# Kernel tuning notes

Measured on AMD Instinct MI355X. Metric: run time of the kernel, lower is better.

## Reference

```python
import jax, jax.numpy as jnp
import numpy as np

N = 50000      # nodes
E = 800000     # edges
F_IN = 128     # num_features
H = 64         # hidden_dim
G = 64         # graphs in batch
EPS = 1e-5


def setup_inputs() -> dict:
    ks = jax.random.split(jax.random.key(0), 16)
    x = jax.random.normal(ks[0], (N, F_IN), dtype=jnp.float32)
    edge_index = jax.random.randint(ks[1], (2, E), 0, N, dtype=jnp.int64)
    batch = jnp.sort(jax.random.randint(ks[2], (N,), 0, G, dtype=jnp.int64))
    s = 0.05
    inp = {"x": x, "edge_index": edge_index, "batch": batch}
    # GCNConv layers: W [out,in], bias [out]; BatchNorm gamma/beta [H]
    dims = [(H, F_IN), (H, H), (H, H)]
    for i, (o, ci) in enumerate(dims):
        inp[f"W{i}"] = jax.random.normal(ks[3 + i], (o, ci), dtype=jnp.float32) * s
        inp[f"b{i}"] = jnp.zeros((o,), dtype=jnp.float32)
        inp[f"g{i}"] = jnp.ones((o,), dtype=jnp.float32)
        inp[f"be{i}"] = jnp.zeros((o,), dtype=jnp.float32)
    inp["lin1_w"] = jax.random.normal(ks[10], (H // 2, H), dtype=jnp.float32) * s
    inp["lin1_b"] = jnp.zeros((H // 2,), dtype=jnp.float32)
    inp["lin2_w"] = jax.random.normal(ks[11], (1, H // 2), dtype=jnp.float32) * s
    inp["lin2_b"] = jnp.zeros((1,), dtype=jnp.float32)
    return inp


def _gcn_conv(x, src, dst, W, b):
    # PyG GCNConv: h = x W^T; add self-loops; symmetric deg^{-1/2} norm; scatter-add; + bias
    h = x @ W.T                                   # [N, out]
    n = x.shape[0]
    deg = jax.ops.segment_sum(jnp.ones(src.shape[0], h.dtype), dst, num_segments=n) + 1.0
    dinv = jax.lax.rsqrt(deg)                     # [N]
    msg = h[src] * (dinv[src] * dinv[dst])[:, None]   # per-edge messages
    agg = jax.ops.segment_sum(msg, dst, num_segments=n)
    agg = agg + h * (dinv * dinv)[:, None]        # self-loop contribution
    return agg + b


def _bn_relu(x, g, be):
    # BatchNorm1d (training-mode batch stats, biased var) + ReLU; dropout = identity (eval)
    m = x.mean(axis=0)
    v = jnp.var(x, axis=0)
    return jax.nn.relu((x - m) * jax.lax.rsqrt(v + EPS) * g + be)


def reference(x, edge_index, batch,
              W0, b0, g0, be0, W1, b1, g1, be1, W2, b2, g2, be2,
              lin1_w, lin1_b, lin2_w, lin2_b):
    src, dst = edge_index[0], edge_index[1]
    Ws = [(W0, b0, g0, be0), (W1, b1, g1, be1), (W2, b2, g2, be2)]
    h = x
    for (W, b, g, be) in Ws:
        h = _bn_relu(_gcn_conv(h, src, dst, W, b), g, be)
    # global mean pool over graphs
    sums = jax.ops.segment_sum(h, batch, num_segments=G)          # [G, H]
    cnt = jax.ops.segment_sum(jnp.ones((h.shape[0],), h.dtype), batch, num_segments=G)
    pooled = sums / jnp.maximum(cnt, 1.0)[:, None]
    h = jax.nn.relu(pooled @ lin1_w.T + lin1_b)
    return h @ lin2_w.T + lin2_b                                   # [G, 1]
```

## Files before the change

### kernel.cpp

```cpp
#include <hip/hip_runtime.h>

#define NN 50000
#define NE 800000
#define FIN 128
#define H 64
#define NG 64
#define BN_EPS 1e-5f
#define INV_N (1.0f / 50000.0f)
#define NBKT 196

__global__ void setup_misc(const float* __restrict__ W0, const float* __restrict__ W1,
                           const float* __restrict__ W2, float* __restrict__ Wt0,
                           float* __restrict__ Wt1, float* __restrict__ Wt2,
                           float* __restrict__ sl0, float* __restrict__ sl1,
                           float* __restrict__ sl2, float* __restrict__ poolcnt,
                           int* __restrict__ bktcnt) {
    int i = blockIdx.x * 256 + threadIdx.x;
    if (i < 64 * 128) { sl0[i] = 0.f; sl1[i] = 0.f; sl2[i] = 0.f; }
    if (i < NG * H + NG) poolcnt[i] = 0.f;
    if (i < NBKT) bktcnt[i] = 0;
    if (i < FIN * 64) {
        int k = i >> 6, o = i & 63;
        Wt0[i] = W0[o * FIN + k];
    }
    if (i < H * 64) {
        int k = i >> 6, o = i & 63;
        Wt1[i] = W1[o * H + k];
        Wt2[i] = W2[o * H + k];
    }
}

__global__ void bucket_hist(const int* __restrict__ dst, int* __restrict__ bktcnt, int E) {
    __shared__ int cnt[NBKT];
    const int chunk = (E + gridDim.x - 1) / gridDim.x;
    const int e0 = blockIdx.x * chunk;
    const int e1 = min(e0 + chunk, E);
    for (int i = threadIdx.x; i < NBKT; i += 256) cnt[i] = 0;
    __syncthreads();
    for (int e = e0 + threadIdx.x; e < e1; e += 256) atomicAdd(&cnt[dst[e] >> 8], 1);
    __syncthreads();
    for (int i = threadIdx.x; i < NBKT; i += 256)
        if (cnt[i]) atomicAdd(&bktcnt[i], cnt[i]);
}

__global__ void bucket_scan(const int* __restrict__ bktcnt, int* __restrict__ bb,
                            int* __restrict__ bcur, int E) {
    __shared__ int s[256];
    int v = (threadIdx.x < NBKT) ? bktcnt[threadIdx.x] : 0;
    s[threadIdx.x] = v;
    __syncthreads();
    for (int off = 1; off < 256; off <<= 1) {
        int t = (threadIdx.x >= off) ? s[threadIdx.x - off] : 0;
        __syncthreads();
        s[threadIdx.x] += t;
        __syncthreads();
    }
    if (threadIdx.x < NBKT) {
        int base = s[threadIdx.x] - v;
        bb[threadIdx.x] = base;
        bcur[threadIdx.x] = base;
    }
    if (threadIdx.x == 0) bb[NBKT] = E;
}

__global__ void bin_edges(const int* __restrict__ src, const int* __restrict__ dst,
                          int* __restrict__ bcur, unsigned int* __restrict__ staged, int E) {
    __shared__ int cnt[NBKT];
    __shared__ int offs[NBKT];
    const int chunk = (E + gridDim.x - 1) / gridDim.x;
    const int e0 = blockIdx.x * chunk;
    const int e1 = min(e0 + chunk, E);
    for (int i = threadIdx.x; i < NBKT; i += 256) cnt[i] = 0;
    __syncthreads();
    for (int e = e0 + threadIdx.x; e < e1; e += 256) atomicAdd(&cnt[dst[e] >> 8], 1);
    __syncthreads();
    for (int i = threadIdx.x; i < NBKT; i += 256) {
        int c = cnt[i];
        offs[i] = c ? atomicAdd(&bcur[i], c) : 0;
        cnt[i] = 0;
    }
    __syncthreads();
    for (int e = e0 + threadIdx.x; e < e1; e += 256) {
        int d = dst[e];
        int bkt = d >> 8;
        int idx = atomicAdd(&cnt[bkt], 1);
        staged[offs[bkt] + idx] = (unsigned int)src[e] | ((unsigned int)(d & 255) << 16);
    }
}

__global__ void csr_build(const unsigned int* __restrict__ staged, const int* __restrict__ bb,
                          int* __restrict__ row_start, float* __restrict__ dinv,
                          int* __restrict__ csr_src, int n, int E) {
    __shared__ int cnt[256];
    __shared__ int loc[256];
    __shared__ int cur[256];
    const int b = blockIdx.x;
    cnt[threadIdx.x] = 0;
    __syncthreads();
    const int e0 = bb[b], e1 = bb[b + 1];
    for (int e = e0 + threadIdx.x; e < e1; e += 256)
        atomicAdd(&cnt[(staged[e] >> 16) & 255], 1);
    __syncthreads();
    int v = cnt[threadIdx.x];
    loc[threadIdx.x] = v;
    __syncthreads();
    for (int off = 1; off < 256; off <<= 1) {
        int t = (threadIdx.x >= off) ? loc[threadIdx.x - off] : 0;
        __syncthreads();
        loc[threadIdx.x] += t;
        __syncthreads();
    }
    const int start = e0 + loc[threadIdx.x] - v;
    const int node = b * 256 + threadIdx.x;
    if (node < n) {
        row_start[node] = start;
        dinv[node] = rsqrtf((float)v + 1.0f);
    }
    if (node == n) row_start[n] = E;
    cur[threadIdx.x] = start;
    __syncthreads();
    for (int e = e0 + threadIdx.x; e < e1; e += 256) {
        unsigned int u = staged[e];
        int j = atomicAdd(&cur[(u >> 16) & 255], 1);
        csr_src[j] = (int)(u & 0xFFFFu);
    }
}

template <int K>
__global__ __launch_bounds__(256, 4) void matmul_tile(const float* __restrict__ x,
                                                      const float* __restrict__ Wtg,
                                                      const float* __restrict__ st,
                                                      const float* __restrict__ gamma,
                                                      const float* __restrict__ beta,
                                                      float* __restrict__ out, int n) {
    __shared__ float Xs[64 * 68];
    __shared__ float Ws[64 * 64];
    const int base = blockIdx.x * 64;
    const int q = threadIdx.x >> 4;
    const int co = (threadIdx.x & 15) * 4;

    float4 a0 = make_float4(0.f, 0.f, 0.f, 0.f);
    float4 a1 = a0, a2 = a0, a3 = a0;

    for (int kc = 0; kc < K; kc += 64) {
        if (kc) __syncthreads();
        for (int i = threadIdx.x; i < 64 * 64; i += 256) Ws[i] = Wtg[kc * 64 + i];
        {
            const int kq = (threadIdx.x & 15) * 4;
            float4 sc = make_float4(1.f, 1.f, 1.f, 1.f);
            float4 sh = make_float4(0.f, 0.f, 0.f, 0.f);
            if (st) {
                int kk = kc + kq;
                float4 s = *(const float4*)&st[kk];
                float4 ss = *(const float4*)&st[64 + kk];
                float4 gm = *(const float4*)&gamma[kk];
                float4 bt = *(const float4*)&beta[kk];
                float mx = s.x * INV_N, my = s.y * INV_N, mz = s.z * INV_N, mw = s.w * INV_N;
                sc.x = gm.x * rsqrtf(ss.x * INV_N - mx * mx + BN_EPS);
                sc.y = gm.y * rsqrtf(ss.y * INV_N - my * my + BN_EPS);
                sc.z = gm.z * rsqrtf(ss.z * INV_N - mz * mz + BN_EPS);
                sc.w = gm.w * rsqrtf(ss.w * INV_N - mw * mw + BN_EPS);
                sh.x = bt.x - mx * sc.x;
                sh.y = bt.y - my * sc.y;
                sh.z = bt.z - mz * sc.z;
                sh.w = bt.w - mw * sc.w;
            }
            for (int j = 0; j < 4; ++j) {
                int r = (threadIdx.x >> 4) + j * 16;
                int row = base + r;
                float4 v = make_float4(0.f, 0.f, 0.f, 0.f);
                if (row < n) v = *(const float4*)&x[(size_t)row * K + kc + kq];
                if (st) {
                    v.x = fmaxf(v.x * sc.x + sh.x, 0.f);
                    v.y = fmaxf(v.y * sc.y + sh.y, 0.f);
                    v.z = fmaxf(v.z * sc.z + sh.z, 0.f);
                    v.w = fmaxf(v.w * sc.w + sh.w, 0.f);
                }
                *(float4*)&Xs[r * 68 + kq] = v;
            }
        }
        __syncthreads();

#pragma unroll 2
        for (int k = 0; k < 64; k += 4) {
            float4 x0 = *(const float4*)&Xs[(q + 0) * 68 + k];
            float4 x1 = *(const float4*)&Xs[(q + 16) * 68 + k];
            float4 x2 = *(const float4*)&Xs[(q + 32) * 68 + k];
            float4 x3 = *(const float4*)&Xs[(q + 48) * 68 + k];
            float4 w0 = *(const float4*)&Ws[(k + 0) * 64 + co];
            float4 w1 = *(const float4*)&Ws[(k + 1) * 64 + co];
            float4 w2 = *(const float4*)&Ws[(k + 2) * 64 + co];
            float4 w3 = *(const float4*)&Ws[(k + 3) * 64 + co];

            a0.x += x0.x * w0.x + x0.y * w1.x + x0.z * w2.x + x0.w * w3.x;
            a0.y += x0.x * w0.y + x0.y * w1.y + x0.z * w2.y + x0.w * w3.y;
            a0.z += x0.x * w0.z + x0.y * w1.z + x0.z * w2.z + x0.w * w3.z;
            a0.w += x0.x * w0.w + x0.y * w1.w + x0.z * w2.w + x0.w * w3.w;

            a1.x += x1.x * w0.x + x1.y * w1.x + x1.z * w2.x + x1.w * w3.x;
            a1.y += x1.x * w0.y + x1.y * w1.y + x1.z * w2.y + x1.w * w3.y;
            a1.z += x1.x * w0.z + x1.y * w1.z + x1.z * w2.z + x1.w * w3.z;
            a1.w += x1.x * w0.w + x1.y * w1.w + x1.z * w2.w + x1.w * w3.w;

            a2.x += x2.x * w0.x + x2.y * w1.x + x2.z * w2.x + x2.w * w3.x;
            a2.y += x2.x * w0.y + x2.y * w1.y + x2.z * w2.y + x2.w * w3.y;
            a2.z += x2.x * w0.z + x2.y * w1.z + x2.z * w2.z + x2.w * w3.z;
            a2.w += x2.x * w0.w + x2.y * w1.w + x2.z * w2.w + x2.w * w3.w;

            a3.x += x3.x * w0.x + x3.y * w1.x + x3.z * w2.x + x3.w * w3.x;
            a3.y += x3.x * w0.y + x3.y * w1.y + x3.z * w2.y + x3.w * w3.y;
            a3.z += x3.x * w0.z + x3.y * w1.z + x3.z * w2.z + x3.w * w3.z;
            a3.w += x3.x * w0.w + x3.y * w1.w + x3.z * w2.w + x3.w * w3.w;
        }
    }

    int r0 = base + q;
    if (r0 < n) *(float4*)&out[(size_t)r0 * H + co] = a0;
    if (r0 + 16 < n) *(float4*)&out[(size_t)(r0 + 16) * H + co] = a1;
    if (r0 + 32 < n) *(float4*)&out[(size_t)(r0 + 32) * H + co] = a2;
    if (r0 + 48 < n) *(float4*)&out[(size_t)(r0 + 48) * H + co] = a3;
}

__global__ void gcn_gather(const float* __restrict__ h, const int* __restrict__ row_start,
                           const int* __restrict__ csr_src, const float* __restrict__ dinv,
                           const float* __restrict__ bias, float* __restrict__ out,
                           float* __restrict__ slots, int n) {
    const int wv = threadIdx.x >> 6;
    const int c = threadIdx.x & 63;
    const int d0 = blockIdx.x * 8 + wv * 2;
    float vA = 0.f, vB = 0.f;
    if (d0 < n) {
        const int d1 = d0 + 1;
        int jA = row_start[d0];
        const int jm = row_start[d1];
        const int je = row_start[d1 + 1];
        int jB = jm;
        float diA = dinv[d0], diB = dinv[d1];
        float bA = h[(size_t)d0 * H + c] * diA * diA + bias[c];
        float bB = h[(size_t)d1 * H + c] * diB * diB + bias[c];
        float a0 = 0.f, a1 = 0.f, a2 = 0.f, a3 = 0.f;
        float b0 = 0.f, b1 = 0.f, b2 = 0.f, b3 = 0.f;
        while (jA + 4 <= jm && jB + 4 <= je) {
            int sA0 = csr_src[jA + 0], sA1 = csr_src[jA + 1];
            int sA2 = csr_src[jA + 2], sA3 = csr_src[jA + 3];
            int sB0 = csr_src[jB + 0], sB1 = csr_src[jB + 1];
            int sB2 = csr_src[jB + 2], sB3 = csr_src[jB + 3];
            float wA0 = dinv[sA0], wA1 = dinv[sA1], wA2 = dinv[sA2], wA3 = dinv[sA3];
            float wB0 = dinv[sB0], wB1 = dinv[sB1], wB2 = dinv[sB2], wB3 = dinv[sB3];
            a0 += h[(size_t)sA0 * H + c] * wA0;
            a1 += h[(size_t)sA1 * H + c] * wA1;
            a2 += h[(size_t)sA2 * H + c] * wA2;
            a3 += h[(size_t)sA3 * H + c] * wA3;
            b0 += h[(size_t)sB0 * H + c] * wB0;
            b1 += h[(size_t)sB1 * H + c] * wB1;
            b2 += h[(size_t)sB2 * H + c] * wB2;
            b3 += h[(size_t)sB3 * H + c] * wB3;
            jA += 4;
            jB += 4;
        }
        for (; jA + 4 <= jm; jA += 4) {
            int s0 = csr_src[jA + 0], s1 = csr_src[jA + 1];
            int s2 = csr_src[jA + 2], s3 = csr_src[jA + 3];
            float w0 = dinv[s0], w1 = dinv[s1], w2 = dinv[s2], w3 = dinv[s3];
            a0 += h[(size_t)s0 * H + c] * w0;
            a1 += h[(size_t)s1 * H + c] * w1;
            a2 += h[(size_t)s2 * H + c] * w2;
            a3 += h[(size_t)s3 * H + c] * w3;
        }
        for (; jA < jm; ++jA) {
            int s = csr_src[jA];
            a0 += h[(size_t)s * H + c] * dinv[s];
        }
        for (; jB + 4 <= je; jB += 4) {
            int s0 = csr_src[jB + 0], s1 = csr_src[jB + 1];
            int s2 = csr_src[jB + 2], s3 = csr_src[jB + 3];
            float w0 = dinv[s0], w1 = dinv[s1], w2 = dinv[s2], w3 = dinv[s3];
            b0 += h[(size_t)s0 * H + c] * w0;
            b1 += h[(size_t)s1 * H + c] * w1;
            b2 += h[(size_t)s2 * H + c] * w2;
            b3 += h[(size_t)s3 * H + c] * w3;
        }
        for (; jB < je; ++jB) {
            int s = csr_src[jB];
            b0 += h[(size_t)s * H + c] * dinv[s];
        }
        vA = bA + diA * ((a0 + a1) + (a2 + a3));
        vB = bB + diB * ((b0 + b1) + (b2 + b3));
        out[(size_t)d0 * H + c] = vA;
        out[(size_t)d1 * H + c] = vB;
    }
    __shared__ float ls[256], lq[256];
    ls[threadIdx.x] = vA + vB;
    lq[threadIdx.x] = vA * vA + vB * vB;
    __syncthreads();
    if (wv == 0) {
        float s = ls[c] + ls[c + 64] + ls[c + 128] + ls[c + 192];
        float q = lq[c] + lq[c + 64] + lq[c + 128] + lq[c + 192];
        float* slot = slots + (blockIdx.x & 63) * 128;
        atomicAdd(&slot[c], s);
        atomicAdd(&slot[64 + c], q);
    }
}

__global__ void reduce_slots(const float* __restrict__ slots, float* __restrict__ st) {
    int c = threadIdx.x;
    float s0 = 0.f, s1 = 0.f, s2 = 0.f, s3 = 0.f;
    for (int k = 0; k < 64; k += 4) {
        s0 += slots[(k + 0) * 128 + c];
        s1 += slots[(k + 1) * 128 + c];
        s2 += slots[(k + 2) * 128 + c];
        s3 += slots[(k + 3) * 128 + c];
    }
    st[c] = (s0 + s1) + (s2 + s3);
}

#define PROWS 16
__global__ void pool_seg(const float* __restrict__ h, const float* __restrict__ st,
                         const float* __restrict__ gamma, const float* __restrict__ beta,
                         const int* __restrict__ batch, float* __restrict__ pool,
                         float* __restrict__ cnt, int n) {
    int wave = blockIdx.x * 4 + (threadIdx.x >> 6);
    int c = threadIdx.x & 63;
    int r0 = wave * PROWS;
    if (r0 >= n) return;
    int r1 = min(r0 + PROWS, n);
    float mean = st[c] * INV_N;
    float var = st[64 + c] * INV_N - mean * mean;
    float sc = gamma[c] * rsqrtf(var + BN_EPS);
    float sh = beta[c] - mean * sc;
    int cur = batch[r0];
    float acc = 0.f;
    int nlocal = 0;
    for (int r = r0; r < r1; ++r) {
        int g = batch[r];
        if (g != cur) {
            atomicAdd(&pool[cur * H + c], acc);
            if (c == 0) atomicAdd(&cnt[cur], (float)nlocal);
            cur = g;
            acc = 0.f;
            nlocal = 0;
        }
        acc += fmaxf(h[(size_t)r * H + c] * sc + sh, 0.f);
        ++nlocal;
    }
    atomicAdd(&pool[cur * H + c], acc);
    if (c == 0) atomicAdd(&cnt[cur], (float)nlocal);
}

__global__ void final_mlp(const float* __restrict__ pool, const float* __restrict__ cnt,
                          const float* __restrict__ l1w, const float* __restrict__ l1b,
                          const float* __restrict__ l2w, const float* __restrict__ l2b,
                          float* __restrict__ out) {
    int tid = blockIdx.x * 256 + threadIdx.x;
    int g = tid >> 5;
    int j = tid & 31;
    if (g >= NG) return;
    float inv = 1.0f / fmaxf(cnt[g], 1.0f);
    float s = l1b[j];
    for (int k = 0; k < H; ++k) s += pool[g * H + k] * inv * l1w[j * H + k];
    float v = fmaxf(s, 0.0f) * l2w[j];
    for (int off = 16; off > 0; off >>= 1) v += __shfl_down(v, off, 32);
    if (j == 0) out[g] = v + l2b[0];
}

extern "C" void kernel_launch(void* const* d_in, const int* in_sizes, int n_in,
                              void* d_out, int out_size, void* d_ws, size_t ws_size,
                              hipStream_t stream) {
    const float* x = (const float*)d_in[0];
    const int* ei = (const int*)d_in[1];
    const int* batch = (const int*)d_in[2];
    const float* W[3] = {(const float*)d_in[3], (const float*)d_in[7], (const float*)d_in[11]};
    const float* b[3] = {(const float*)d_in[4], (const float*)d_in[8], (const float*)d_in[12]};
    const float* g[3] = {(const float*)d_in[5], (const float*)d_in[9], (const float*)d_in[13]};
    const float* be[3] = {(const float*)d_in[6], (const float*)d_in[10], (const float*)d_in[14]};
    const float* l1w = (const float*)d_in[15];
    const float* l1b = (const float*)d_in[16];
    const float* l2w = (const float*)d_in[17];
    const float* l2b = (const float*)d_in[18];
    float* out = (float*)d_out;

    const int* src = ei;
    const int* dst = ei + NE;

    char* wsb = (char*)d_ws;
    size_t off = 0;
    auto alloc = [&](size_t elems) {
        void* p = wsb + off;
        off += elems * 4;
        return p;
    };
    float* dinv = (float*)alloc(50048);
    float* bufA = (float*)alloc((size_t)NN * H);
    float* bufB = (float*)alloc((size_t)NN * H);
    float* slots[3] = {(float*)alloc(64 * 128), (float*)alloc(64 * 128), (float*)alloc(64 * 128)};
    float* st[3] = {(float*)alloc(128), (float*)alloc(128), (float*)alloc(128)};
    float* pool = (float*)alloc(NG * H);
    float* cnt = (float*)alloc(64);
    float* Wt[3] = {(float*)alloc(FIN * 64), (float*)alloc(H * 64), (float*)alloc(H * 64)};
    int* row_start = (int*)alloc(50112);
    int* bktcnt = (int*)alloc(256);
    int* bb = (int*)alloc(256);
    int* bcur = (int*)alloc(256);
    unsigned int* staged = (unsigned int*)alloc(NE);
    int* csr_src = (int*)alloc(NE);

    setup_misc<<<32, 256, 0, stream>>>(W[0], W[1], W[2], Wt[0], Wt[1], Wt[2], slots[0], slots[1],
                                       slots[2], pool, bktcnt);
    bucket_hist<<<256, 256, 0, stream>>>(dst, bktcnt, NE);
    bucket_scan<<<1, 256, 0, stream>>>(bktcnt, bb, bcur, NE);
    bin_edges<<<256, 256, 0, stream>>>(src, dst, bcur, staged, NE);
    csr_build<<<NBKT, 256, 0, stream>>>(staged, bb, row_start, dinv, csr_src, NN, NE);

    const int grid_mm = (NN + 63) / 64;
    const int grid_gather = (NN + 7) / 8;

    for (int L = 0; L < 3; ++L) {
        if (L == 0)
            matmul_tile<FIN><<<grid_mm, 256, 0, stream>>>(x, Wt[0], nullptr, nullptr, nullptr,
                                                          bufA, NN);
        else
            matmul_tile<H><<<grid_mm, 256, 0, stream>>>(bufB, Wt[L], st[L - 1], g[L - 1],
                                                        be[L - 1], bufA, NN);
        gcn_gather<<<grid_gather, 256, 0, stream>>>(bufA, row_start, csr_src, dinv, b[L], bufB,
                                                    slots[L], NN);
        reduce_slots<<<1, 128, 0, stream>>>(slots[L], st[L]);
    }

    const int pool_waves = (NN + PROWS - 1) / PROWS;
    pool_seg<<<(pool_waves + 3) / 4, 256, 0, stream>>>(bufB, st[2], g[2], be[2], batch, pool,
                                                       cnt, NN);
    final_mlp<<<8, 256, 0, stream>>>(pool, cnt, l1w, l1b, l2w, l2b, out);
}
```

Baseline: 344.7 us.

## Fold tail reductions into producer kernels via last-block ticket counters

Removes the separate bucket_scan, reduce_slots and final_mlp launches. Each producer kernel now takes an atomic ticket, and the last block to finish does the scan, the slot reduction or the final MLP itself. This cuts five small serial kernel launches and their launch gaps. In exchange every block pays a threadfence plus an atomic, and the tail work runs on a single block, reading the shared data through atomic loads.

Result: slower. 862.9 us (+150.3%).

```diff
diff --git a/kernel.cpp b/kernel.cpp
--- a/kernel.cpp
+++ b/kernel.cpp
@@ -14,11 +14,12 @@
                            float* __restrict__ Wt1, float* __restrict__ Wt2,
                            float* __restrict__ sl0, float* __restrict__ sl1,
                            float* __restrict__ sl2, float* __restrict__ poolcnt,
-                           int* __restrict__ bktcnt) {
+                           int* __restrict__ bktcnt, int* __restrict__ tickets) {
     int i = blockIdx.x * 256 + threadIdx.x;
     if (i < 64 * 128) { sl0[i] = 0.f; sl1[i] = 0.f; sl2[i] = 0.f; }
     if (i < NG * H + NG) poolcnt[i] = 0.f;
     if (i < NBKT) bktcnt[i] = 0;
+    if (i < 8) tickets[i] = 0;
     if (i < FIN * 64) {
         int k = i >> 6, o = i & 63;
         Wt0[i] = W0[o * FIN + k];
@@ -30,8 +31,12 @@
     }
 }
 
-__global__ void bucket_hist(const int* __restrict__ dst, int* __restrict__ bktcnt, int E) {
+__global__ void bucket_hist(const int* __restrict__ dst, int* __restrict__ bktcnt,
+                            int* __restrict__ bb, int* __restrict__ bcur,
+                            int* __restrict__ ticket, int E) {
     __shared__ int cnt[NBKT];
+    __shared__ int s[256];
+    __shared__ int is_last;
     const int chunk = (E + gridDim.x - 1) / gridDim.x;
     const int e0 = blockIdx.x * chunk;
     const int e1 = min(e0 + chunk, E);
@@ -41,26 +46,29 @@
     __syncthreads();
     for (int i = threadIdx.x; i < NBKT; i += 256)
         if (cnt[i]) atomicAdd(&bktcnt[i], cnt[i]);
-}
-
-__global__ void bucket_scan(const int* __restrict__ bktcnt, int* __restrict__ bb,
-                            int* __restrict__ bcur, int E) {
-    __shared__ int s[256];
-    int v = (threadIdx.x < NBKT) ? bktcnt[threadIdx.x] : 0;
-    s[threadIdx.x] = v;
-    __syncthreads();
-    for (int off = 1; off < 256; off <<= 1) {
-        int t = (threadIdx.x >= off) ? s[threadIdx.x - off] : 0;
+    __syncthreads();
+    if (threadIdx.x == 0) {
+        __threadfence();
+        is_last = (atomicAdd(ticket, 1) == (int)gridDim.x - 1);
+    }
+    __syncthreads();
+    if (is_last) {
+        int v = (threadIdx.x < NBKT) ? atomicAdd(&bktcnt[threadIdx.x], 0) : 0;
+        s[threadIdx.x] = v;
         __syncthreads();
-        s[threadIdx.x] += t;
-        __syncthreads();
-    }
-    if (threadIdx.x < NBKT) {
-        int base = s[threadIdx.x] - v;
-        bb[threadIdx.x] = base;
-        bcur[threadIdx.x] = base;
-    }
-    if (threadIdx.x == 0) bb[NBKT] = E;
+        for (int off = 1; off < 256; off <<= 1) {
+            int t = (threadIdx.x >= off) ? s[threadIdx.x - off] : 0;
+            __syncthreads();
+            s[threadIdx.x] += t;
+            __syncthreads();
+        }
+        if (threadIdx.x < NBKT) {
+            int base = s[threadIdx.x] - v;
+            bb[threadIdx.x] = base;
+            bcur[threadIdx.x] = base;
+        }
+        if (threadIdx.x == 0) bb[NBKT] = E;
+    }
 }
 
 __global__ void bin_edges(const int* __restrict__ src, const int* __restrict__ dst,
@@ -224,7 +232,8 @@
 __global__ void gcn_gather(const float* __restrict__ h, const int* __restrict__ row_start,
                            const int* __restrict__ csr_src, const float* __restrict__ dinv,
                            const float* __restrict__ bias, float* __restrict__ out,
-                           float* __restrict__ slots, int n) {
+                           float* __restrict__ slots, float* __restrict__ st,
+                           int* __restrict__ ticket, int n) {
     const int wv = threadIdx.x >> 6;
     const int c = threadIdx.x & 63;
     const int d0 = blockIdx.x * 8 + wv * 2;
@@ -290,6 +299,7 @@
         out[(size_t)d1 * H + c] = vB;
     }
     __shared__ float ls[256], lq[256];
+    __shared__ int is_last;
     ls[threadIdx.x] = vA + vB;
     lq[threadIdx.x] = vA * vA + vB * vB;
     __syncthreads();
@@ -300,67 +310,86 @@
         atomicAdd(&slot[c], s);
         atomicAdd(&slot[64 + c], q);
     }
-}
-
-__global__ void reduce_slots(const float* __restrict__ slots, float* __restrict__ st) {
-    int c = threadIdx.x;
-    float s0 = 0.f, s1 = 0.f, s2 = 0.f, s3 = 0.f;
-    for (int k = 0; k < 64; k += 4) {
-        s0 += slots[(k + 0) * 128 + c];
-        s1 += slots[(k + 1) * 128 + c];
-        s2 += slots[(k + 2) * 128 + c];
-        s3 += slots[(k + 3) * 128 + c];
-    }
-    st[c] = (s0 + s1) + (s2 + s3);
+    __syncthreads();
+    if (threadIdx.x == 0) {
+        __threadfence();
+        is_last = (atomicAdd(ticket, 1) == (int)gridDim.x - 1);
+    }
+    __syncthreads();
+    if (is_last && threadIdx.x < 128) {
+        int cc = threadIdx.x;
+        float s = 0.f;
+        for (int k = 0; k < 64; ++k) s += atomicAdd(&slots[k * 128 + cc], 0.0f);
+        st[cc] = s;
+    }
 }
 
 #define PROWS 16
 __global__ void pool_seg(const float* __restrict__ h, const float* __restrict__ st,
                          const float* __restrict__ gamma, const float* __restrict__ beta,
                          const int* __restrict__ batch, float* __restrict__ pool,
-                         float* __restrict__ cnt, int n) {
+                         float* __restrict__ cnt, const float* __restrict__ l1w,
+                         const float* __restrict__ l1b, const float* __restrict__ l2w,
+                         const float* __restrict__ l2b, float* __restrict__ out,
+                         int* __restrict__ ticket, int n) {
     int wave = blockIdx.x * 4 + (threadIdx.x >> 6);
     int c = threadIdx.x & 63;
     int r0 = wave * PROWS;
-    if (r0 >= n) return;
-    int r1 = min(r0 + PROWS, n);
-    float mean = st[c] * INV_N;
-    float var = st[64 + c] * INV_N - mean * mean;
-    float sc = gamma[c] * rsqrtf(var + BN_EPS);
-    float sh = beta[c] - mean * sc;
-    int cur = batch[r0];
-    float acc = 0.f;
-    int nlocal = 0;
-    for (int r = r0; r < r1; ++r) {
-        int g = batch[r];
-        if (g != cur) {
-            atomicAdd(&pool[cur * H + c], acc);
-            if (c == 0) atomicAdd(&cnt[cur], (float)nlocal);
-            cur = g;
-            acc = 0.f;
-            nlocal = 0;
-        }
-        acc += fmaxf(h[(size_t)r * H + c] * sc + sh, 0.f);
-        ++nlocal;
-    }
-    atomicAdd(&pool[cur * H + c], acc);
-    if (c == 0) atomicAdd(&cnt[cur], (float)nlocal);
-}
-
-__global__ void final_mlp(const float* __restrict__ pool, const float* __restrict__ cnt,
-                          const float* __restrict__ l1w, const float* __restrict__ l1b,
-                          const float* __restrict__ l2w, const float* __restrict__ l2b,
-                          float* __restrict__ out) {
-    int tid = blockIdx.x * 256 + threadIdx.x;
-    int g = tid >> 5;
-    int j = tid & 31;
-    if (g >= NG) return;
-    float inv = 1.0f / fmaxf(cnt[g], 1.0f);
-    float s = l1b[j];
-    for (int k = 0; k < H; ++k) s += pool[g * H + k] * inv * l1w[j * H + k];
-    float v = fmaxf(s, 0.0f) * l2w[j];
-    for (int off = 16; off > 0; off >>= 1) v += __shfl_down(v, off, 32);
-    if (j == 0) out[g] = v + l2b[0];
+    if (r0 < n) {
+        int r1 = min(r0 + PROWS, n);
+        float mean = st[c] * INV_N;
+        float var = st[64 + c] * INV_N - mean * mean;
+        float sc = gamma[c] * rsqrtf(var + BN_EPS);
+        float sh = beta[c] - mean * sc;
+        int cur = batch[r0];
+        float acc = 0.f;
+        int nlocal = 0;
+        for (int r = r0; r < r1; ++r) {
+            int g = batch[r];
+            if (g != cur) {
+                atomicAdd(&pool[cur * H + c], acc);
+                if (c == 0) atomicAdd(&cnt[cur], (float)nlocal);
+                cur = g;
+                acc = 0.f;
+                nlocal = 0;
+            }
+            acc += fmaxf(h[(size_t)r * H + c] * sc + sh, 0.f);
+            ++nlocal;
+        }
+        atomicAdd(&pool[cur * H + c], acc);
+        if (c == 0) atomicAdd(&cnt[cur], (float)nlocal);
+    }
+    __shared__ int is_last;
+    __syncthreads();
+    if (threadIdx.x == 0) {
+        __threadfence();
+        is_last = (atomicAdd(ticket, 1) == (int)gridDim.x - 1);
+    }
+    __syncthreads();
+    if (!is_last) return;
+    __shared__ float ps[NG * H];
+    __shared__ float partial[256];
+    __shared__ float cinv[NG];
+    if (threadIdx.x < NG) cinv[threadIdx.x] = 1.0f / fmaxf(atomicAdd(&cnt[threadIdx.x], 0.0f), 1.0f);
+    __syncthreads();
+    for (int i = threadIdx.x; i < NG * H; i += 256)
+        ps[i] = atomicAdd(&pool[i], 0.0f) * cinv[i >> 6];
+    __syncthreads();
+    {
+        int gg = threadIdx.x & 63;
+        int part = threadIdx.x >> 6;
+        float acc = 0.f;
+        for (int j = part * 8; j < part * 8 + 8; ++j) {
+            float s = l1b[j];
+            for (int k = 0; k < H; ++k) s += ps[gg * H + k] * l1w[j * H + k];
+            acc += fmaxf(s, 0.0f) * l2w[j];
+        }
+        partial[threadIdx.x] = acc;
+        __syncthreads();
+        if (part == 0)
+            out[gg] = l2b[0] + ((partial[gg] + partial[gg + 64]) +
+                                (partial[gg + 128] + partial[gg + 192]));
+    }
 }
 
 extern "C" void kernel_launch(void* const* d_in, const int* in_sizes, int n_in,
@@ -401,13 +430,13 @@
     int* bktcnt = (int*)alloc(256);
     int* bb = (int*)alloc(256);
     int* bcur = (int*)alloc(256);
+    int* tickets = (int*)alloc(8);
     unsigned int* staged = (unsigned int*)alloc(NE);
     int* csr_src = (int*)alloc(NE);
 
     setup_misc<<<32, 256, 0, stream>>>(W[0], W[1], W[2], Wt[0], Wt[1], Wt[2], slots[0], slots[1],
-                                       slots[2], pool, bktcnt);
-    bucket_hist<<<256, 256, 0, stream>>>(dst, bktcnt, NE);
-    bucket_scan<<<1, 256, 0, stream>>>(bktcnt, bb, bcur, NE);
+                                       slots[2], pool, bktcnt, tickets);
+    bucket_hist<<<256, 256, 0, stream>>>(dst, bktcnt, bb, bcur, &tickets[0], NE);
     bin_edges<<<256, 256, 0, stream>>>(src, dst, bcur, staged, NE);
     csr_build<<<NBKT, 256, 0, stream>>>(staged, bb, row_start, dinv, csr_src, NN, NE);
 
@@ -422,12 +451,11 @@
             matmul_tile<H><<<grid_mm, 256, 0, stream>>>(bufB, Wt[L], st[L - 1], g[L - 1],
                                                         be[L - 1], bufA, NN);
         gcn_gather<<<grid_gather, 256, 0, stream>>>(bufA, row_start, csr_src, dinv, b[L], bufB,
-                                                    slots[L], NN);
-        reduce_slots<<<1, 128, 0, stream>>>(slots[L], st[L]);
+                                                    slots[L], st[L], &tickets[1 + L], NN);
     }
 
     const int pool_waves = (NN + PROWS - 1) / PROWS;
     pool_seg<<<(pool_waves + 3) / 4, 256, 0, stream>>>(bufB, st[2], g[2], be[2], batch, pool,
-                                                       cnt, NN);
-    final_mlp<<<8, 256, 0, stream>>>(pool, cnt, l1w, l1b, l2w, l2b, out);
-}
+                                                       cnt, l1w, l1b, l2w, l2b, out,
+                                                       &tickets[4], NN);
+}
```
